# Kernel optimization log

Measured on AMD Instinct MI355X. Metric: run time of the kernel, lower is better.

Reference implementation:

```python
import jax, jax.numpy as jnp
import numpy as np


def setup_inputs() -> dict:
    key = jax.random.key(0)
    k1, k2, k3 = jax.random.split(key, 3)
    dim = 512
    x = jax.random.normal(k1, (8, dim, 64, 64), dtype=jnp.float32)
    # 1x1 convs with bias=False are channel matmuls: weight[out_ch, in_ch]
    w_qkv = jax.random.normal(k2, (3 * dim, dim), dtype=jnp.float32) * (dim ** -0.5)
    w_out = jax.random.normal(k3, (dim, dim), dtype=jnp.float32) * (dim ** -0.5)
    return {"x": x, "w_qkv": w_qkv, "w_out": w_out}


def reference(x, w_qkv, w_out):
    b, c, h, w = x.shape
    n = h * w
    scale = c ** -0.5
    xf = x.reshape(b, c, n)                          # b c (h w)
    qkv = jnp.einsum('oc,bcn->bon', w_qkv, xf)       # 1x1 conv QKV projection
    q, k, v = jnp.split(qkv, 3, axis=1)              # each [b, c, n]
    score = jnp.einsum('bcq,bck->bqk', q * scale, k) # full N x N attention
    attn = jax.nn.softmax(score, axis=-1)
    out = jnp.einsum('bqk,bck->bcq', attn, v)        # [b, c, n]
    out = jnp.einsum('oc,bcn->bon', w_out, out)      # 1x1 conv out projection
    return out.reshape(b, c, h, w)
```

## Files before the change

kernel.cpp:

```cpp
#include <hip/hip_runtime.h>
#include <hip/hip_bf16.h>


typedef __bf16 bf16x8 __attribute__((ext_vector_type(8)));
typedef float f32x4 __attribute__((ext_vector_type(4)));
typedef __hip_bfloat16 bf16_t;

#define BM 128
#define BN 128
#define BKT 64

static __device__ __forceinline__ void glds16(const void* g, void* l) {
  __builtin_amdgcn_global_load_lds(
      (__attribute__((address_space(1))) const void*)g,
      (__attribute__((address_space(3))) void*)l, 16, 0, 0);
}

template <int MODE>
__global__ void __launch_bounds__(256, 2)
gemm_bt(const bf16_t* __restrict__ A, long long strideA, int lda,
        const bf16_t* __restrict__ Bt, long long strideB, int ldb,
        void* __restrict__ Cv, long long strideC, int ldc,
        int K, float scale,
        float* __restrict__ rowsum, int strideRS) {
  __shared__ char sA[2][BM * BKT * 2];
  __shared__ char sB[2][BN * BKT * 2];

  const int tid = threadIdx.x;
  const int lane = tid & 63;
  const int wid = tid >> 6;
  const int wm = wid >> 1, wn = wid & 1;
  const int lr = lane & 15, lk = lane >> 4;
  const int b = blockIdx.z;

  const char* Ab = (const char*)(A + (long long)b * strideA + (size_t)blockIdx.x * BM * lda);
  const char* Bb = (const char*)(Bt + (long long)b * strideB + (size_t)blockIdx.y * BN * ldb);
  const size_t ldab = (size_t)lda * 2, ldbb = (size_t)ldb * 2;

  auto stage = [&](int buf, int k0) {
#pragma unroll
    for (int c = 0; c < 4; ++c) {
      const int obase = wid * 4096 + c * 1024;
      const int o = obase + lane * 16;
      const int row = o >> 7;
      const int kb = (o & 127) ^ ((row & 7) << 4);
      glds16(Ab + (size_t)row * ldab + (size_t)k0 * 2 + kb, &sA[buf][obase]);
      glds16(Bb + (size_t)row * ldbb + (size_t)k0 * 2 + kb, &sB[buf][obase]);
    }
  };

  const int nt = K / BKT;
  f32x4 acc[4][4] = {};

  stage(0, 0);
  asm volatile("s_waitcnt vmcnt(0)" ::: "memory");
  __builtin_amdgcn_s_barrier();

  for (int t = 0; t < nt; ++t) {
    if (t + 1 < nt) stage((t + 1) & 1, (t + 1) * BKT);
    const char* cA = sA[t & 1];
    const char* cB = sB[t & 1];
#pragma unroll
    for (int kk = 0; kk < 2; ++kk) {
      const int kb = (kk * 64 + lk * 16) ^ ((lr & 7) << 4);
      bf16x8 av[4], bv[4];
#pragma unroll
      for (int f = 0; f < 4; ++f) {
        av[f] = *(const bf16x8*)(cA + (((wm * 64 + f * 16 + lr) << 7) + kb));
        bv[f] = *(const bf16x8*)(cB + (((wn * 64 + f * 16 + lr) << 7) + kb));
      }
#pragma unroll
      for (int fm = 0; fm < 4; ++fm)
#pragma unroll
        for (int fn = 0; fn < 4; ++fn)
          acc[fm][fn] = __builtin_amdgcn_mfma_f32_16x16x32_bf16(av[fm], bv[fn], acc[fm][fn], 0, 0, 0);
    }
    asm volatile("s_waitcnt vmcnt(0)" ::: "memory");
    __builtin_amdgcn_s_barrier();
  }

  const int mbase = blockIdx.x * BM + wm * 64;
  const int nbase = blockIdx.y * BN + wn * 64;

  if (MODE == 0) {
    bf16_t* C = (bf16_t*)Cv + (long long)b * strideC;
#pragma unroll
    for (int fm = 0; fm < 4; ++fm)
#pragma unroll
      for (int fn = 0; fn < 4; ++fn)
#pragma unroll
        for (int r = 0; r < 4; ++r) {
          const int row = mbase + fm * 16 + lk * 4 + r;
          const int col = nbase + fn * 16 + lr;
          C[(size_t)row * ldc + col] = __float2bfloat16(acc[fm][fn][r]);
        }
  } else if (MODE == 2) {
    bf16_t* P = (bf16_t*)Cv + (long long)b * strideC;
    float* rs = rowsum + (long long)b * strideRS;
#pragma unroll
    for (int fm = 0; fm < 4; ++fm)
#pragma unroll
      for (int r = 0; r < 4; ++r) {
        const int row = mbase + fm * 16 + lk * 4 + r;
        float s = 0.f;
#pragma unroll
        for (int fn = 0; fn < 4; ++fn) {
          const float v = __expf(acc[fm][fn][r] * scale);
          const int col = nbase + fn * 16 + lr;
          P[(size_t)row * ldc + col] = __float2bfloat16(v);
          s += v;
        }
        s += __shfl_xor(s, 1);
        s += __shfl_xor(s, 2);
        s += __shfl_xor(s, 4);
        s += __shfl_xor(s, 8);
        if (lr == 0) atomicAdd(&rs[row], s);
      }
  } else {
    float* O = (float*)Cv + (long long)b * strideC;
    const float* rs = rowsum + (long long)b * strideRS;
#pragma unroll
    for (int fn = 0; fn < 4; ++fn) {
      const int col = nbase + fn * 16 + lr;
      const float inv = 1.0f / rs[col];
#pragma unroll
      for (int fm = 0; fm < 4; ++fm)
#pragma unroll
        for (int r = 0; r < 4; ++r) {
          const int row = mbase + fm * 16 + lk * 4 + r;
          O[(size_t)row * ldc + col] = acc[fm][fn][r] * inv;
        }
    }
  }
}

__global__ void cast_f32_bf16(const float* __restrict__ in, bf16_t* __restrict__ out, int n) {
  const int i = blockIdx.x * blockDim.x + threadIdx.x;
  if (i < n) out[i] = __float2bfloat16(in[i]);
}

__global__ void zero_f32(float* __restrict__ p, int n) {
  const int i = blockIdx.x * blockDim.x + threadIdx.x;
  if (i < n) p[i] = 0.f;
}

__global__ void transpose_cast(const float* __restrict__ x, bf16_t* __restrict__ xT) {
  __shared__ float t[32][33];
  const int b = blockIdx.z;
  const int n0 = blockIdx.x * 32, c0 = blockIdx.y * 32;
  const int tx = threadIdx.x & 31, ty = threadIdx.x >> 5;
  const float* xb = x + (size_t)b * (512 * 4096);
#pragma unroll
  for (int i = 0; i < 32; i += 8)
    t[ty + i][tx] = xb[(size_t)(c0 + ty + i) * 4096 + n0 + tx];
  __syncthreads();
  bf16_t* xo = xT + (size_t)b * (4096 * 512);
#pragma unroll
  for (int i = 0; i < 32; i += 8)
    xo[(size_t)(n0 + ty + i) * 512 + c0 + tx] = __float2bfloat16(t[tx][ty + i]);
}

__global__ void transpose_cast_512(const float* __restrict__ in, bf16_t* __restrict__ out) {
  __shared__ float t[32][33];
  const int r0 = blockIdx.x * 32, c0 = blockIdx.y * 32;
  const int tx = threadIdx.x & 31, ty = threadIdx.x >> 5;
#pragma unroll
  for (int i = 0; i < 32; i += 8)
    t[ty + i][tx] = in[(size_t)(r0 + ty + i) * 512 + c0 + tx];
  __syncthreads();
#pragma unroll
  for (int i = 0; i < 32; i += 8)
    out[(size_t)(c0 + ty + i) * 512 + r0 + tx] = __float2bfloat16(t[tx][ty + i]);
}

extern "C" void kernel_launch(void* const* d_in, const int* in_sizes, int n_in,
                              void* d_out, int out_size, void* d_ws, size_t ws_size,
                              hipStream_t stream) {
  const float* x = (const float*)d_in[0];
  const float* wqkv = (const float*)d_in[1];
  const float* wout = (const float*)d_in[2];
  char* ws = (char*)d_ws;

  const size_t o_qkT = 0;
  const size_t o_U   = 67108864ull;
  const size_t o_wqk = 100663296ull;
  const size_t o_wo  = 101711872ull;
  const size_t o_wvT = 102236160ull;
  const size_t o_wov = 102760448ull;
  const size_t o_rs  = 103284736ull;
  const size_t o_xT  = 103415808ull;

  bf16_t* qkT = (bf16_t*)(ws + o_qkT);
  bf16_t* U   = (bf16_t*)(ws + o_U);
  bf16_t* wqkb = (bf16_t*)(ws + o_wqk);
  bf16_t* wob  = (bf16_t*)(ws + o_wo);
  bf16_t* wvT  = (bf16_t*)(ws + o_wvT);
  bf16_t* wov  = (bf16_t*)(ws + o_wov);
  float*  rs   = (float*)(ws + o_rs);
  bf16_t* xT   = (bf16_t*)(ws + o_xT);
  bf16_t* P    = (bf16_t*)(ws + o_xT);

  const size_t pbytes = 33554432ull;
  const size_t avail = ws_size > o_xT ? ws_size - o_xT : 0;
  int chunk = 1;
  if (avail >= 8 * pbytes) chunk = 8;
  else if (avail >= 4 * pbytes) chunk = 4;
  else if (avail >= 2 * pbytes) chunk = 2;

  const float scale = 0.04419417382415922f;

  cast_f32_bf16<<<2048, 256, 0, stream>>>(wqkv, wqkb, 524288);
  cast_f32_bf16<<<1024, 256, 0, stream>>>(wout, wob, 262144);
  transpose_cast_512<<<dim3(16, 16), 256, 0, stream>>>(wqkv + 524288, wvT);
  zero_f32<<<128, 256, 0, stream>>>(rs, 32768);
  transpose_cast<<<dim3(128, 16, 8), 256, 0, stream>>>(x, xT);

  gemm_bt<0><<<dim3(32, 8, 8), 256, 0, stream>>>(
      xT, 2097152LL, 512, wqkb, 0LL, 512, qkT, 4194304LL, 1024, 512, 1.f, nullptr, 0);

  gemm_bt<0><<<dim3(4, 4, 1), 256, 0, stream>>>(
      wob, 0LL, 512, wvT, 0LL, 512, wov, 0LL, 512, 512, 1.f, nullptr, 0);

  gemm_bt<0><<<dim3(4, 32, 8), 256, 0, stream>>>(
      wov, 0LL, 512, xT, 2097152LL, 512, U, 2097152LL, 4096, 512, 1.f, nullptr, 0);

  for (int cb = 0; cb < 8; cb += chunk) {
    gemm_bt<2><<<dim3(32, 32, chunk), 256, 0, stream>>>(
        qkT + (size_t)cb * 4194304, 4194304LL, 1024,
        qkT + (size_t)cb * 4194304 + 512, 4194304LL, 1024,
        P, 16777216LL, 4096, 512, scale, rs + cb * 4096, 4096);
    gemm_bt<5><<<dim3(4, 32, chunk), 256, 0, stream>>>(
        U + (size_t)cb * 2097152, 2097152LL, 4096,
        P, 16777216LL, 4096,
        (float*)d_out + (size_t)cb * 2097152, 2097152LL, 4096,
        4096, 1.f, rs + cb * 4096, 4096);
  }
}
```

Measured before the change: 618.4 us.

## Replace GEMM with 256x256-tile eight-wave kernel using interleaved quadrant pipeline

Rewrites the shared batched GEMM to use 256x256 output tiles with 512 threads (8 waves) and a 128 KB LDS buffer. The K loop now runs in 128-wide steps, split into quadrant phases. LDS reads for one quadrant, global-to-LDS loads for the next stage and MFMA blocks on another quadrant are interleaved, with fine-grained waitcnt/barrier control and s_setprio raised around the MFMA runs. The aim is higher arithmetic intensity per LDS byte and better overlap of memory traffic with matrix math. In exchange, grids become coarser (some launches have few blocks per CU), LDS use limits occupancy to about one block per CU, and there are many more barriers.

New measurement: 636.9 us. 1.03x slower.

```diff
diff --git a/kernel.cpp b/kernel.cpp
--- a/kernel.cpp
+++ b/kernel.cpp
@@ -5,10 +5,6 @@
 typedef __bf16 bf16x8 __attribute__((ext_vector_type(8)));
 typedef float f32x4 __attribute__((ext_vector_type(4)));
 typedef __hip_bfloat16 bf16_t;
-
-#define BM 128
-#define BN 128
-#define BKT 64
 
 static __device__ __forceinline__ void glds16(const void* g, void* l) {
   __builtin_amdgcn_global_load_lds(
@@ -16,98 +12,135 @@
       (__attribute__((address_space(3))) void*)l, 16, 0, 0);
 }
 
+#define BAR asm volatile("s_barrier" ::: "memory")
+#define LGKM0 asm volatile("s_waitcnt lgkmcnt(0)" ::: "memory")
+#define LGKM8 asm volatile("s_waitcnt lgkmcnt(8)" ::: "memory")
+#define VM0 asm volatile("s_waitcnt vmcnt(0)" ::: "memory")
+#define VM2 asm volatile("s_waitcnt vmcnt(2)" ::: "memory")
+
+#define READ_A(buf, qm)                                                       \
+  {                                                                           \
+    const int rgA = (((buf)*2 + wm) << 14);                                   \
+    _Pragma("unroll") for (int j = 0; j < 4; ++j) {                           \
+      const int ro = rgA + ((((qm)*4 + j)*16 + lr) << 7);                     \
+      _Pragma("unroll") for (int kk = 0; kk < 2; ++kk)                        \
+        av[j][kk] = *(const bf16x8*)(lds + ro + ((kk*64 + lk*16) ^ swz));     \
+    }                                                                         \
+  }
+#define READ_B(buf, qn)                                                       \
+  {                                                                           \
+    const int rgB = 65536 + (((buf)*2 + bh) << 14) + bsub;                    \
+    _Pragma("unroll") for (int n = 0; n < 2; ++n) {                           \
+      const int ro = rgB + ((((qn)*2 + n)*16 + lr) << 7);                     \
+      _Pragma("unroll") for (int kk = 0; kk < 2; ++kk)                        \
+        bv[n][kk] = *(const bf16x8*)(lds + ro + ((kk*64 + lk*16) ^ swz));     \
+    }                                                                         \
+  }
+#define MFMA_Q(qm, qn)                                                        \
+  __builtin_amdgcn_s_setprio(1);                                              \
+  _Pragma("unroll") for (int j = 0; j < 4; ++j)                               \
+    _Pragma("unroll") for (int n = 0; n < 2; ++n)                             \
+      _Pragma("unroll") for (int kk = 0; kk < 2; ++kk)                        \
+        acc[(qm)*4 + j][(qn)*2 + n] =                                         \
+            __builtin_amdgcn_mfma_f32_16x16x32_bf16(                          \
+                av[j][kk], bv[n][kk], acc[(qm)*4 + j][(qn)*2 + n], 0, 0, 0);  \
+  __builtin_amdgcn_s_setprio(0);
+
 template <int MODE>
-__global__ void __launch_bounds__(256, 2)
-gemm_bt(const bf16_t* __restrict__ A, long long strideA, int lda,
-        const bf16_t* __restrict__ Bt, long long strideB, int ldb,
-        void* __restrict__ Cv, long long strideC, int ldc,
-        int K, float scale,
-        float* __restrict__ rowsum, int strideRS) {
-  __shared__ char sA[2][BM * BKT * 2];
-  __shared__ char sB[2][BN * BKT * 2];
-
+__global__ void __launch_bounds__(512, 2)
+gemm8(const bf16_t* __restrict__ A, long long strideA, int lda,
+      const bf16_t* __restrict__ Bt, long long strideB, int ldb,
+      void* __restrict__ Cv, long long strideC, int ldc,
+      int K, float scale, float* __restrict__ rowsum, int strideRS) {
+  __shared__ char lds[131072];
   const int tid = threadIdx.x;
   const int lane = tid & 63;
   const int wid = tid >> 6;
-  const int wm = wid >> 1, wn = wid & 1;
+  const int wm = wid >> 2, wn = wid & 3;
   const int lr = lane & 15, lk = lane >> 4;
+  const int swz = (lr & 7) << 4;
+  const int bh = wn >> 1, bsub = (wn & 1) << 13;
   const int b = blockIdx.z;
 
-  const char* Ab = (const char*)(A + (long long)b * strideA + (size_t)blockIdx.x * BM * lda);
-  const char* Bb = (const char*)(Bt + (long long)b * strideB + (size_t)blockIdx.y * BN * ldb);
-  const size_t ldab = (size_t)lda * 2, ldbb = (size_t)ldb * 2;
-
-  auto stage = [&](int buf, int k0) {
-#pragma unroll
-    for (int c = 0; c < 4; ++c) {
-      const int obase = wid * 4096 + c * 1024;
-      const int o = obase + lane * 16;
-      const int row = o >> 7;
-      const int kb = (o & 127) ^ ((row & 7) << 4);
-      glds16(Ab + (size_t)row * ldab + (size_t)k0 * 2 + kb, &sA[buf][obase]);
-      glds16(Bb + (size_t)row * ldbb + (size_t)k0 * 2 + kb, &sB[buf][obase]);
+  const char* Ab = (const char*)(A + (long long)b*strideA + (size_t)blockIdx.x*256*lda);
+  const char* Bb = (const char*)(Bt + (long long)b*strideB + (size_t)blockIdx.y*256*ldb);
+  const size_t ldab = (size_t)lda*2, ldbb = (size_t)ldb*2;
+
+  auto stage = [&](int m, int buf, int half, int kt) {
+    const char* src = m ? Bb : Ab;
+    const size_t ld = m ? ldbb : ldab;
+    char* dst = lds + (m << 16) + ((buf*2 + half) << 14);
+#pragma unroll
+    for (int c = 0; c < 2; ++c) {
+      const int oin = wid*2048 + c*1024 + lane*16;
+      const int row = half*128 + (oin >> 7);
+      const int kb = (oin & 127) ^ (((oin >> 7) & 7) << 4);
+      glds16(src + (size_t)row*ld + (size_t)kt*128 + kb, dst + wid*2048 + c*1024);
     }
   };
 
-  const int nt = K / BKT;
-  f32x4 acc[4][4] = {};
-
-  stage(0, 0);
-  asm volatile("s_waitcnt vmcnt(0)" ::: "memory");
-  __builtin_amdgcn_s_barrier();
-
-  for (int t = 0; t < nt; ++t) {
-    if (t + 1 < nt) stage((t + 1) & 1, (t + 1) * BKT);
-    const char* cA = sA[t & 1];
-    const char* cB = sB[t & 1];
-#pragma unroll
-    for (int kk = 0; kk < 2; ++kk) {
-      const int kb = (kk * 64 + lk * 16) ^ ((lr & 7) << 4);
-      bf16x8 av[4], bv[4];
-#pragma unroll
-      for (int f = 0; f < 4; ++f) {
-        av[f] = *(const bf16x8*)(cA + (((wm * 64 + f * 16 + lr) << 7) + kb));
-        bv[f] = *(const bf16x8*)(cB + (((wn * 64 + f * 16 + lr) << 7) + kb));
-      }
-#pragma unroll
-      for (int fm = 0; fm < 4; ++fm)
-#pragma unroll
-        for (int fn = 0; fn < 4; ++fn)
-          acc[fm][fn] = __builtin_amdgcn_mfma_f32_16x16x32_bf16(av[fm], bv[fn], acc[fm][fn], 0, 0, 0);
-    }
-    asm volatile("s_waitcnt vmcnt(0)" ::: "memory");
-    __builtin_amdgcn_s_barrier();
-  }
-
-  const int mbase = blockIdx.x * BM + wm * 64;
-  const int nbase = blockIdx.y * BN + wn * 64;
+  f32x4 acc[8][4] = {};
+  bf16x8 av[4][2], bv[2][2];
+  const int niter = K >> 7;
+
+  stage(0,0,0,0); stage(0,0,1,0); stage(1,0,0,0); stage(1,0,1,0);
+  stage(0,1,0,1);
+  VM2; BAR;
+
+  for (int i = 0; i < niter; ++i) {
+    const bool nl = (i + 1 < niter);
+    const int o1 = 2*i + 1, e2 = 2*i + 2, o3 = 2*i + 3;
+    READ_A(0,0); READ_B(0,0); stage(0,1,1,o1);
+    LGKM8; BAR; LGKM0; MFMA_Q(0,0); BAR;
+    READ_B(0,1); stage(1,1,0,o1);
+    BAR; LGKM0; MFMA_Q(0,1); BAR;
+    READ_A(0,1); stage(1,1,1,o1);
+    BAR; LGKM0; MFMA_Q(1,1); BAR;
+    READ_B(0,0); if (nl) stage(0,0,0,e2);
+    BAR; LGKM0; MFMA_Q(1,0);
+    if (nl) { VM2; } else { VM0; }
+    BAR;
+    READ_A(1,0); READ_B(1,0); if (nl) stage(0,0,1,e2);
+    LGKM8; BAR; LGKM0; MFMA_Q(0,0); BAR;
+    READ_B(1,1); if (nl) stage(1,0,0,e2);
+    BAR; LGKM0; MFMA_Q(0,1); BAR;
+    READ_A(1,1); if (nl) stage(1,0,1,e2);
+    BAR; LGKM0; MFMA_Q(1,1); BAR;
+    READ_B(1,0); if (nl) stage(0,1,0,o3);
+    BAR; LGKM0; MFMA_Q(1,0);
+    if (nl) { VM2; }
+    BAR;
+  }
+
+  const int mbase = blockIdx.x*256 + wm*128;
+  const int nbase = blockIdx.y*256 + wn*64;
 
   if (MODE == 0) {
     bf16_t* C = (bf16_t*)Cv + (long long)b * strideC;
 #pragma unroll
-    for (int fm = 0; fm < 4; ++fm)
+    for (int fm = 0; fm < 8; ++fm)
 #pragma unroll
       for (int fn = 0; fn < 4; ++fn)
 #pragma unroll
         for (int r = 0; r < 4; ++r) {
-          const int row = mbase + fm * 16 + lk * 4 + r;
-          const int col = nbase + fn * 16 + lr;
-          C[(size_t)row * ldc + col] = __float2bfloat16(acc[fm][fn][r]);
+          const int row = mbase + fm*16 + lk*4 + r;
+          const int col = nbase + fn*16 + lr;
+          C[(size_t)row*ldc + col] = __float2bfloat16(acc[fm][fn][r]);
         }
   } else if (MODE == 2) {
     bf16_t* P = (bf16_t*)Cv + (long long)b * strideC;
     float* rs = rowsum + (long long)b * strideRS;
 #pragma unroll
-    for (int fm = 0; fm < 4; ++fm)
+    for (int fm = 0; fm < 8; ++fm)
 #pragma unroll
       for (int r = 0; r < 4; ++r) {
-        const int row = mbase + fm * 16 + lk * 4 + r;
+        const int row = mbase + fm*16 + lk*4 + r;
         float s = 0.f;
 #pragma unroll
         for (int fn = 0; fn < 4; ++fn) {
           const float v = __expf(acc[fm][fn][r] * scale);
-          const int col = nbase + fn * 16 + lr;
-          P[(size_t)row * ldc + col] = __float2bfloat16(v);
+          const int col = nbase + fn*16 + lr;
+          P[(size_t)row*ldc + col] = __float2bfloat16(v);
           s += v;
         }
         s += __shfl_xor(s, 1);
@@ -121,14 +154,14 @@
     const float* rs = rowsum + (long long)b * strideRS;
 #pragma unroll
     for (int fn = 0; fn < 4; ++fn) {
-      const int col = nbase + fn * 16 + lr;
+      const int col = nbase + fn*16 + lr;
       const float inv = 1.0f / rs[col];
 #pragma unroll
-      for (int fm = 0; fm < 4; ++fm)
+      for (int fm = 0; fm < 8; ++fm)
 #pragma unroll
         for (int r = 0; r < 4; ++r) {
-          const int row = mbase + fm * 16 + lk * 4 + r;
-          O[(size_t)row * ldc + col] = acc[fm][fn][r] * inv;
+          const int row = mbase + fm*16 + lk*4 + r;
+          O[(size_t)row*ldc + col] = acc[fm][fn][r] * inv;
         }
     }
   }
@@ -190,8 +223,8 @@
   const size_t o_rs  = 103284736ull;
   const size_t o_xT  = 103415808ull;
 
-  bf16_t* qkT = (bf16_t*)(ws + o_qkT);
-  bf16_t* U   = (bf16_t*)(ws + o_U);
+  bf16_t* qkT  = (bf16_t*)(ws + o_qkT);
+  bf16_t* U    = (bf16_t*)(ws + o_U);
   bf16_t* wqkb = (bf16_t*)(ws + o_wqk);
   bf16_t* wob  = (bf16_t*)(ws + o_wo);
   bf16_t* wvT  = (bf16_t*)(ws + o_wvT);
@@ -215,21 +248,21 @@
   zero_f32<<<128, 256, 0, stream>>>(rs, 32768);
   transpose_cast<<<dim3(128, 16, 8), 256, 0, stream>>>(x, xT);
 
-  gemm_bt<0><<<dim3(32, 8, 8), 256, 0, stream>>>(
+  gemm8<0><<<dim3(16, 4, 8), 512, 0, stream>>>(
       xT, 2097152LL, 512, wqkb, 0LL, 512, qkT, 4194304LL, 1024, 512, 1.f, nullptr, 0);
 
-  gemm_bt<0><<<dim3(4, 4, 1), 256, 0, stream>>>(
+  gemm8<0><<<dim3(2, 2, 1), 512, 0, stream>>>(
       wob, 0LL, 512, wvT, 0LL, 512, wov, 0LL, 512, 512, 1.f, nullptr, 0);
 
-  gemm_bt<0><<<dim3(4, 32, 8), 256, 0, stream>>>(
+  gemm8<0><<<dim3(2, 16, 8), 512, 0, stream>>>(
       wov, 0LL, 512, xT, 2097152LL, 512, U, 2097152LL, 4096, 512, 1.f, nullptr, 0);
 
   for (int cb = 0; cb < 8; cb += chunk) {
-    gemm_bt<2><<<dim3(32, 32, chunk), 256, 0, stream>>>(
+    gemm8<2><<<dim3(16, 16, chunk), 512, 0, stream>>>(
         qkT + (size_t)cb * 4194304, 4194304LL, 1024,
         qkT + (size_t)cb * 4194304 + 512, 4194304LL, 1024,
         P, 16777216LL, 4096, 512, scale, rs + cb * 4096, 4096);
-    gemm_bt<5><<<dim3(4, 32, chunk), 256, 0, stream>>>(
+    gemm8<5><<<dim3(2, 16, chunk), 512, 0, stream>>>(
         U + (size_t)cb * 2097152, 2097152LL, 4096,
         P, 16777216LL, 4096,
         (float*)d_out + (size_t)cb * 2097152, 2097152LL, 4096,
```
